# Performance work log

Hardware: AMD Instinct MI355X
Metric: run time of the kernel (lower is better)

The kernel has to match this reference:

```python
import jax, jax.numpy as jnp
import numpy as np

MAX_LEN = 3

def _attention(h, enc, w1, b1, w2):
    # h: [B,H], enc: [B,S,H]
    B, S, H = enc.shape
    hs = jnp.broadcast_to(h[:, None, :], (B, S, H))
    x = jnp.tanh(jnp.concatenate([enc, hs], axis=-1) @ w1.T + b1)  # [B,S,H]
    e = (x @ w2.T)[..., 0]                                         # [B,S]
    alpha = jax.nn.softmax(e, axis=1)
    return jnp.einsum('bs,bsd->bd', alpha, enc)                    # [B,H]

def _gru_cell(x, h, w_ih, w_hh, b_ih, b_hh):
    # torch GRU gate order: r, z, n
    H = h.shape[-1]
    gi = x @ w_ih.T + b_ih   # [B,3H]
    gh = h @ w_hh.T + b_hh
    i_r, i_z, i_n = gi[:, :H], gi[:, H:2*H], gi[:, 2*H:]
    h_r, h_z, h_n = gh[:, :H], gh[:, H:2*H], gh[:, 2*H:]
    r = jax.nn.sigmoid(i_r + h_r)
    z = jax.nn.sigmoid(i_z + h_z)
    n = jnp.tanh(i_n + r * h_n)
    return (1.0 - z) * n + z * h

def setup_inputs() -> dict:
    key = jax.random.key(0)
    ks = jax.random.split(key, 16)
    B, S, H, DW = 1024, 40, 1024, 512
    V0 = V1 = 4000
    EMB_N = V0 + V1 + 1
    sc = lambda fan: 1.0 / np.sqrt(fan)
    inp = {
        'encoder_outputs': jax.random.normal(ks[0], (B, S, H), jnp.float32),
        'encoder_hidden': jax.random.normal(ks[1], (1, B, H), jnp.float32),
        'targets': jax.random.randint(ks[2], (MAX_LEN, B), 0, V0),
        'emb': jax.random.normal(ks[3], (EMB_N, DW), jnp.float32) * 0.02,
        'attn_w1': jax.random.normal(ks[4], (H, 2 * H), jnp.float32) * sc(2 * H),
        'attn_b1': jnp.zeros((H,), jnp.float32),
        'attn_w2': jax.random.normal(ks[5], (1, H), jnp.float32) * sc(H),
        'w_ih': jax.random.normal(ks[6], (3 * H, H + DW), jnp.float32) * sc(H),
        'w_hh': jax.random.normal(ks[7], (3 * H, H), jnp.float32) * sc(H),
        'b_ih': jnp.zeros((3 * H,), jnp.float32),
        'b_hh': jnp.zeros((3 * H,), jnp.float32),
        'out0_w': jax.random.normal(ks[8], (V0, H), jnp.float32) * sc(H),
        'out0_b': jnp.zeros((V0,), jnp.float32),
        'out1_w': jax.random.normal(ks[9], (V1, H), jnp.float32) * sc(H),
        'out1_b': jnp.zeros((V1,), jnp.float32),
    }
    return inp

def reference(encoder_outputs, encoder_hidden, targets, emb, attn_w1, attn_b1,
              attn_w2, w_ih, w_hh, b_ih, b_hh, out0_w, out0_b, out1_w, out1_b):
    B = encoder_outputs.shape[0]
    h = encoder_hidden[0]  # n_layers=1, unidirectional -> init state passthrough
    logs = []
    for t in range(MAX_LEN):
        context = _attention(h, encoder_outputs, attn_w1, attn_b1, attn_w2)
        if t == 0:
            it = jnp.zeros((B,), jnp.int32)
        elif t == 1:
            it = targets[0] + 1
        else:
            it = targets[t - 1] + 36
        x = jnp.concatenate([emb[it], context], axis=1)  # [B, DW+H]
        h = _gru_cell(x, h, w_ih, w_hh, b_ih, b_hh)
        if t == 0 or t == 2:
            logits = h @ out0_w.T + out0_b
        else:
            logits = h @ out1_w.T + out1_b
        logs.append(jax.nn.log_softmax(logits, axis=1))
    return jnp.stack(logs)  # [MAX_LEN, B, V]
```

## Files before the change

kernel.cpp:

```cpp
#include <hip/hip_runtime.h>
#include <hip/hip_bf16.h>
#include <math.h>

#define B_SZ 1024
#define S_SZ 40
#define H_SZ 1024
#define DW_SZ 512
#define V_SZ 4000
#define XW (DW_SZ + H_SZ)
#define NGL 8192

typedef __bf16 bf16x8 __attribute__((ext_vector_type(8)));
typedef float f32x4 __attribute__((ext_vector_type(4)));
typedef unsigned short u16x8 __attribute__((ext_vector_type(8)));

__device__ __forceinline__ float fast_tanh(float x) {
    return 1.0f - 2.0f / (1.0f + __expf(2.0f * x));
}
__device__ __forceinline__ float fast_sigmoid(float x) {
    return 1.0f / (1.0f + __expf(-x));
}
__device__ __forceinline__ float bfraw2f(unsigned short u) {
    return __uint_as_float(((unsigned)u) << 16);
}
__device__ __forceinline__ ushort4 cvt4(float4 v) {
    union { ushort4 u; __hip_bfloat16 h[4]; } o;
    o.h[0] = __float2bfloat16(v.x); o.h[1] = __float2bfloat16(v.y);
    o.h[2] = __float2bfloat16(v.z); o.h[3] = __float2bfloat16(v.w);
    return o.u;
}
__device__ __forceinline__ u16x8 pack8(float4 a, float4 b) {
    union { u16x8 v; ushort4 h[2]; } o;
    o.h[0] = cvt4(a); o.h[1] = cvt4(b);
    return o.v;
}

#define GLL16(gp, lp)                                                                \
    __builtin_amdgcn_global_load_lds((const __attribute__((address_space(1))) void*)(gp), \
                                     (__attribute__((address_space(3))) void*)(lp), 16, 0, 0)

__device__ void cast_tail_block(int blk, int tid,
                                const float* __restrict__ w1, const float* __restrict__ whh,
                                const float* __restrict__ wih, const float* __restrict__ o0,
                                const float* __restrict__ o1,
                                __hip_bfloat16* __restrict__ wall0,
                                __hip_bfloat16* __restrict__ wall1,
                                __hip_bfloat16* __restrict__ wih_bf) {
    ushort4* w0u = reinterpret_cast<ushort4*>(wall0);
    ushort4* w1u = reinterpret_cast<ushort4*>(wall1);
    if (blk < 256) {
        const int r0 = blk * 4;
        const float4* s = reinterpret_cast<const float4*>(w1);
        ushort4 u0 = cvt4(s[(r0 + 0) * 512 + 256 + tid]), u1 = cvt4(s[(r0 + 1) * 512 + 256 + tid]),
                u2 = cvt4(s[(r0 + 2) * 512 + 256 + tid]), u3 = cvt4(s[(r0 + 3) * 512 + 256 + tid]);
        const int li = r0 * 256 + tid;
        w0u[li] = u0; w0u[li + 256] = u1; w0u[li + 512] = u2; w0u[li + 768] = u3;
        w1u[li] = u0; w1u[li + 256] = u1; w1u[li + 512] = u2; w1u[li + 768] = u3;
    } else if (blk < 1024) {
        const int li = (blk - 256) * 1024 + tid;
        const float4* s = reinterpret_cast<const float4*>(whh);
        ushort4 u0 = cvt4(s[li]), u1 = cvt4(s[li + 256]), u2 = cvt4(s[li + 512]), u3 = cvt4(s[li + 768]);
        w0u[262144 + li] = u0; w0u[262144 + li + 256] = u1;
        w0u[262144 + li + 512] = u2; w0u[262144 + li + 768] = u3;
        w1u[262144 + li] = u0; w1u[262144 + li + 256] = u1;
        w1u[262144 + li + 512] = u2; w1u[262144 + li + 768] = u3;
    } else if (blk < 2176) {
        const int li = (blk - 1024) * 1024 + tid;
        const float4* s = reinterpret_cast<const float4*>(wih);
        float4 v0 = s[li], v1 = s[li + 256], v2 = s[li + 512], v3 = s[li + 768];
        ushort4* d = reinterpret_cast<ushort4*>(wih_bf);
        d[li] = cvt4(v0); d[li + 256] = cvt4(v1); d[li + 512] = cvt4(v2); d[li + 768] = cvt4(v3);
    } else if (blk < 3176) {
        const int li = (blk - 2176) * 1024 + tid;
        const float4* s = reinterpret_cast<const float4*>(o0);
        float4 v0 = s[li], v1 = s[li + 256], v2 = s[li + 512], v3 = s[li + 768];
        w0u[1048576 + li] = cvt4(v0); w0u[1048576 + li + 256] = cvt4(v1);
        w0u[1048576 + li + 512] = cvt4(v2); w0u[1048576 + li + 768] = cvt4(v3);
    } else if (blk < 4176) {
        const int li = (blk - 3176) * 1024 + tid;
        const float4* s = reinterpret_cast<const float4*>(o1);
        float4 v0 = s[li], v1 = s[li + 256], v2 = s[li + 512], v3 = s[li + 768];
        w1u[1048576 + li] = cvt4(v0); w1u[1048576 + li + 256] = cvt4(v1);
        w1u[1048576 + li + 512] = cvt4(v2); w1u[1048576 + li + 768] = cvt4(v3);
    } else {
        const ushort4 z = make_ushort4(0, 0, 0, 0);
        if (blk < 4200) {
            const int li = 2072576 + (blk - 4176) * 1024 + tid;
            w0u[li] = z; w0u[li + 256] = z; w0u[li + 512] = z; w0u[li + 768] = z;
        } else {
            const int li = 2072576 + (blk - 4200) * 1024 + tid;
            w1u[li] = z; w1u[li + 256] = z; w1u[li + 512] = z; w1u[li + 768] = z;
        }
    }
}

__global__ __launch_bounds__(256, 2) void gemm_enc_cast(
    const __hip_bfloat16* __restrict__ A, int lda,
    const __hip_bfloat16* __restrict__ W, int ldw,
    __hip_bfloat16* __restrict__ C, int ldc,
    int nbx, int K, int gemm_nb,
    const float* __restrict__ w1, const float* __restrict__ whh,
    const float* __restrict__ wih, const float* __restrict__ o0,
    const float* __restrict__ o1,
    __hip_bfloat16* __restrict__ wall0, __hip_bfloat16* __restrict__ wall1,
    __hip_bfloat16* __restrict__ wih_bf) {
    extern __shared__ char smem[];
    const int tid = threadIdx.x;

    if ((int)blockIdx.x >= gemm_nb) {
        cast_tail_block(blockIdx.x - gemm_nb, tid, w1, whh, wih, o0, o1, wall0, wall1, wih_bf);
        return;
    }

    const int lane = tid & 63;
    const int wave = tid >> 6;
    const int wm = wave >> 1, wn = wave & 1;
    const int fr = lane & 15, fq = lane >> 4;

    int bid = blockIdx.x;
    { const int cpx = gemm_nb >> 3; bid = (bid & 7) * cpx + (bid >> 3); }
    const int by = bid / nbx;
    const int bm = by * 128;
    const int bn = (bid - by * nbx) * 256;

    const int r0 = tid >> 2;
    const int s0 = (tid & 3) ^ ((tid >> 3) & 3);
    const __hip_bfloat16* gA0 = A + (size_t)(bm + r0) * lda + s0 * 8;
    const __hip_bfloat16* gA1 = A + (size_t)(bm + r0 + 64) * lda + s0 * 8;
    const __hip_bfloat16* gW0 = W + (size_t)(bn + r0) * ldw + s0 * 8;
    const __hip_bfloat16* gW1 = W + (size_t)(bn + r0 + 64) * ldw + s0 * 8;
    const __hip_bfloat16* gW2 = W + (size_t)(bn + r0 + 128) * ldw + s0 * 8;
    const __hip_bfloat16* gW3 = W + (size_t)(bn + r0 + 192) * ldw + s0 * 8;
    const int dst0 = tid * 16;

    int aoff[4], boff[8];
#pragma unroll
    for (int mi = 0; mi < 4; ++mi) {
        const int row = wm * 64 + mi * 16 + fr;
        aoff[mi] = row * 64 + ((fq ^ ((row >> 1) & 3)) << 4);
    }
#pragma unroll
    for (int ni = 0; ni < 8; ++ni) {
        const int col = wn * 128 + ni * 16 + fr;
        boff[ni] = 8192 + col * 64 + ((fq ^ ((col >> 1) & 3)) << 4);
    }

    const int NT = K >> 5;
    f32x4 acc[4][8] = {};

#define STAGE_T(t)                                                    \
    do {                                                              \
        char* sb = smem + ((t) % 3) * 24576;                          \
        const int kk = (t) << 5;                                      \
        GLL16(gA0 + kk, sb + dst0);                                   \
        GLL16(gA1 + kk, sb + dst0 + 4096);                            \
        GLL16(gW0 + kk, sb + 8192 + dst0);                            \
        GLL16(gW1 + kk, sb + 8192 + dst0 + 4096);                     \
        GLL16(gW2 + kk, sb + 8192 + dst0 + 8192);                     \
        GLL16(gW3 + kk, sb + 8192 + dst0 + 12288);                    \
    } while (0)

    STAGE_T(0);
    STAGE_T(1);
    __builtin_amdgcn_sched_barrier(0);
    asm volatile("s_waitcnt vmcnt(6)" ::: "memory");
    __builtin_amdgcn_s_barrier();
    __builtin_amdgcn_sched_barrier(0);

    for (int t = 0; t < NT; ++t) {
        const char* sb = smem + (t % 3) * 24576;
        bf16x8 af[4], bg[8];
#pragma unroll
        for (int ni = 0; ni < 8; ++ni) bg[ni] = *reinterpret_cast<const bf16x8*>(sb + boff[ni]);
#pragma unroll
        for (int mi = 0; mi < 4; ++mi) af[mi] = *reinterpret_cast<const bf16x8*>(sb + aoff[mi]);

        if (t + 2 < NT) STAGE_T(t + 2);

        __builtin_amdgcn_s_setprio(1);
#pragma unroll
        for (int mi = 0; mi < 4; ++mi)
#pragma unroll
            for (int ni = 0; ni < 8; ++ni)
                acc[mi][ni] = __builtin_amdgcn_mfma_f32_16x16x32_bf16(af[mi], bg[ni], acc[mi][ni], 0, 0, 0);
        __builtin_amdgcn_s_setprio(0);

        if (t != NT - 1) {
            __builtin_amdgcn_sched_barrier(0);
            if (t + 2 < NT) asm volatile("s_waitcnt vmcnt(6)" ::: "memory");
            else            asm volatile("s_waitcnt vmcnt(0)" ::: "memory");
            __builtin_amdgcn_s_barrier();
            __builtin_amdgcn_sched_barrier(0);
        }
    }
#undef STAGE_T

#pragma unroll
    for (int ni = 0; ni < 8; ++ni) {
        const int col = bn + wn * 128 + ni * 16 + fr;
#pragma unroll
        for (int mi = 0; mi < 4; ++mi) {
            const int row0 = bm + wm * 64 + mi * 16 + fq * 4;
#pragma unroll
            for (int r = 0; r < 4; ++r)
                C[(size_t)(row0 + r) * ldc + col] = __float2bfloat16(acc[mi][ni][r]);
        }
    }
}

__global__ __launch_bounds__(512, 2) void gemm_bt_pipe128_v2(
    const __hip_bfloat16* __restrict__ A, int lda,
    const __hip_bfloat16* __restrict__ W, int ldw,
    const float* __restrict__ bias,
    __hip_bfloat16* __restrict__ C, int ldc,
    int nbx, int K) {
    extern __shared__ char smem[];
    const int tid = threadIdx.x;
    const int lane = tid & 63;
    const int wave = tid >> 6;
    const int wm = wave >> 2, wn = wave & 3;
    const int fr = lane & 15, fq = lane >> 4;

    int bid = blockIdx.x;
    { const int cpx = gridDim.x >> 3; bid = (bid & 7) * cpx + (bid >> 3); }
    const int by = bid / nbx;
    const int bm = by * 128;
    const int bn = (bid - by * nbx) * 256;

    const int r0 = tid >> 2;
    const int s0 = (tid & 3) ^ ((tid >> 3) & 3);
    const __hip_bfloat16* gA0 = A + (size_t)(bm + r0) * lda + s0 * 8;
    const __hip_bfloat16* gW0 = W + (size_t)(bn + r0) * ldw + s0 * 8;
    const __hip_bfloat16* gW1 = W + (size_t)(bn + r0 + 128) * ldw + s0 * 8;
    const int dst0 = tid * 16;

    int aoff[4], boff[4];
#pragma unroll
    for (int mi = 0; mi < 4; ++mi) {
        const int row = wm * 64 + mi * 16 + fr;
        aoff[mi] = row * 64 + ((fq ^ ((row >> 1) & 3)) << 4);
    }
#pragma unroll
    for (int ni = 0; ni < 4; ++ni) {
        const int col = wn * 64 + ni * 16 + fr;
        boff[ni] = 8192 + col * 64 + ((fq ^ ((col >> 1) & 3)) << 4);
    }

    const int NT = K >> 5;
    f32x4 acc[4][4] = {};

#define STAGE_T(t)                                                    \
    do {                                                              \
        char* sb = smem + ((t) % 3) * 24576;                          \
        const int kk = (t) << 5;                                      \
        GLL16(gA0 + kk, sb + dst0);                                   \
        GLL16(gW0 + kk, sb + 8192 + dst0);                            \
        GLL16(gW1 + kk, sb + 8192 + dst0 + 8192);                     \
    } while (0)

    STAGE_T(0);
    STAGE_T(1);
    __builtin_amdgcn_sched_barrier(0);
    asm volatile("s_waitcnt vmcnt(3)" ::: "memory");
    __builtin_amdgcn_s_barrier();
    __builtin_amdgcn_sched_barrier(0);

    for (int t = 0; t < NT; ++t) {
        const char* sb = smem + (t % 3) * 24576;
        bf16x8 af[4], bg[4];
#pragma unroll
        for (int ni = 0; ni < 4; ++ni) bg[ni] = *reinterpret_cast<const bf16x8*>(sb + boff[ni]);
#pragma unroll
        for (int mi = 0; mi < 4; ++mi) af[mi] = *reinterpret_cast<const bf16x8*>(sb + aoff[mi]);

        if (t + 2 < NT) STAGE_T(t + 2);

        __builtin_amdgcn_s_setprio(1);
#pragma unroll
        for (int mi = 0; mi < 4; ++mi)
#pragma unroll
            for (int ni = 0; ni < 4; ++ni)
                acc[mi][ni] = __builtin_amdgcn_mfma_f32_16x16x32_bf16(af[mi], bg[ni], acc[mi][ni], 0, 0, 0);
        __builtin_amdgcn_s_setprio(0);

        if (t != NT - 1) {
            __builtin_amdgcn_sched_barrier(0);
            if (t + 2 < NT) asm volatile("s_waitcnt vmcnt(3)" ::: "memory");
            else            asm volatile("s_waitcnt vmcnt(0)" ::: "memory");
            __builtin_amdgcn_s_barrier();
            __builtin_amdgcn_sched_barrier(0);
        }
    }
#undef STAGE_T

#pragma unroll
    for (int ni = 0; ni < 4; ++ni) {
        const int col = bn + wn * 64 + ni * 16 + fr;
        const float bb = bias ? bias[col] : 0.0f;
#pragma unroll
        for (int mi = 0; mi < 4; ++mi) {
            const int row0 = bm + wm * 64 + mi * 16 + fq * 4;
#pragma unroll
            for (int r = 0; r < 4; ++r)
                C[(size_t)(row0 + r) * ldc + col] = __float2bfloat16(acc[mi][ni][r] + bb);
        }
    }
}

#define PA_ENC 10240
#define PA_W1A (PA_ENC + 256)
#define PA_EMB (PA_W1A + 3072)
#define PA_H   (PA_EMB + 1024)
#define PA_TOT (PA_H + 2)
__global__ __launch_bounds__(256) void prep_a_kernel(
    const float* __restrict__ enc, const float* __restrict__ w1,
    __hip_bfloat16* __restrict__ enc_bf, __hip_bfloat16* __restrict__ w1a_bf,
    const float* __restrict__ emb, const int* __restrict__ targets,
    __hip_bfloat16* __restrict__ x0, __hip_bfloat16* __restrict__ x1, __hip_bfloat16* __restrict__ x2,
    const float* __restrict__ enc_h, float* __restrict__ h, __hip_bfloat16* __restrict__ h_bf,
    const float* __restrict__ b1, const float* __restrict__ b_hh,
    const float* __restrict__ o0b, const float* __restrict__ o1b,
    float* __restrict__ bias0, float* __restrict__ bias1) {
    const int blk = blockIdx.x;
    const int tid = threadIdx.x;

    if (blk < PA_ENC) {
        const float4* s = reinterpret_cast<const float4*>(enc);
        u16x8* d = reinterpret_cast<u16x8*>(enc_bf);
        const int f0 = blk * 1024 + tid * 2;
        const int f1 = f0 + 512;
        float4 a0 = s[f0], a1 = s[f0 + 1];
        float4 b0 = s[f1], b1v = s[f1 + 1];
        d[blk * 512 + tid] = pack8(a0, a1);
        d[blk * 512 + 256 + tid] = pack8(b0, b1v);
    } else if (blk < PA_W1A) {
        const int r0 = (blk - PA_ENC) * 4;
        const float4* s = reinterpret_cast<const float4*>(w1);
        float4 v0 = s[(r0 + 0) * 512 + tid], v1 = s[(r0 + 1) * 512 + tid],
               v2 = s[(r0 + 2) * 512 + tid], v3 = s[(r0 + 3) * 512 + tid];
        ushort4* d = reinterpret_cast<ushort4*>(w1a_bf);
        const int li = r0 * 256 + tid;
        d[li] = cvt4(v0); d[li + 256] = cvt4(v1); d[li + 512] = cvt4(v2); d[li + 768] = cvt4(v3);
    } else if (blk < PA_EMB) {
        if (tid >= 128) return;
        const int e = blk - PA_W1A;
        const int t = e >> 10;
        const int b = e & 1023;
        int it; __hip_bfloat16* x;
        if (t == 0) { it = 0; x = x0; }
        else if (t == 1) { it = targets[b] + 1; x = x1; }
        else { it = targets[B_SZ + b] + 36; x = x2; }
        float4 v = reinterpret_cast<const float4*>(emb + (size_t)it * DW_SZ)[tid];
        reinterpret_cast<ushort4*>(x + (size_t)b * XW)[tid] = cvt4(v);
    } else if (blk < PA_H) {
        const int i = (blk - PA_EMB) * 256 + tid;
        const float4 v = reinterpret_cast<const float4*>(enc_h)[i];
        reinterpret_cast<float4*>(h)[i] = v;
        reinterpret_cast<ushort4*>(h_bf)[i] = cvt4(v);
    } else {
        float* bt = (blk == PA_H) ? bias0 : bias1;
        const float* ob = (blk == PA_H) ? o0b : o1b;
        for (int j = tid; j < NGL; j += 256) {
            float v;
            if (j < H_SZ) v = b1[j];
            else if (j < 4 * H_SZ) v = b_hh[j - H_SZ];
            else if (j < 4 * H_SZ + V_SZ) v = ob[j - 4 * H_SZ];
            else v = 0.0f;
            bt[j] = v;
        }
    }
}

__global__ __launch_bounds__(256) void attn_ls_kernel(
    const __hip_bfloat16* __restrict__ enc,
    const __hip_bfloat16* __restrict__ enc_proj,
    const __hip_bfloat16* __restrict__ hgl,
    const float* __restrict__ w2,
    __hip_bfloat16* __restrict__ x,
    float* __restrict__ outp,
    int nattn) {
    const int blk = blockIdx.x;
    const int tid = threadIdx.x;
    const int lane = tid & 63, wave = tid >> 6;
    __shared__ float s_e[S_SZ];
    __shared__ float s_red[4];
    __shared__ float s_bc;

    if (blk < nattn) {
        const int b = blk;
        float hp[16], wv[16];
        const unsigned short* hgrow = reinterpret_cast<const unsigned short*>(hgl) + (size_t)b * NGL;
#pragma unroll
        for (int p = 0; p < 4; ++p) {
            const int base = p * 256 + lane * 4;
            ushort4 hu = *reinterpret_cast<const ushort4*>(hgrow + base);
            float4 wq = *reinterpret_cast<const float4*>(w2 + base);
            hp[p * 4 + 0] = bfraw2f(hu.x); hp[p * 4 + 1] = bfraw2f(hu.y);
            hp[p * 4 + 2] = bfraw2f(hu.z); hp[p * 4 + 3] = bfraw2f(hu.w);
            wv[p * 4 + 0] = wq.x; wv[p * 4 + 1] = wq.y;
            wv[p * 4 + 2] = wq.z; wv[p * 4 + 3] = wq.w;
        }

        const unsigned short* ep0 = reinterpret_cast<const unsigned short*>(enc_proj) + (size_t)b * S_SZ * H_SZ;
#pragma unroll 2
        for (int i = 0; i < 10; ++i) {
            const int s = wave + 4 * i;
            const unsigned short* row = ep0 + (size_t)s * H_SZ;
            float acc = 0.f;
#pragma unroll
            for (int p = 0; p < 4; ++p) {
                ushort4 eu = *reinterpret_cast<const ushort4*>(row + p * 256 + lane * 4);
                acc += fast_tanh(bfraw2f(eu.x) + hp[p * 4 + 0]) * wv[p * 4 + 0]
                     + fast_tanh(bfraw2f(eu.y) + hp[p * 4 + 1]) * wv[p * 4 + 1]
                     + fast_tanh(bfraw2f(eu.z) + hp[p * 4 + 2]) * wv[p * 4 + 2]
                     + fast_tanh(bfraw2f(eu.w) + hp[p * 4 + 3]) * wv[p * 4 + 3];
            }
#pragma unroll
            for (int off = 32; off > 0; off >>= 1) acc += __shfl_down(acc, off);
            if (lane == 0) s_e[s] = acc;
        }
        __syncthreads();

        float m = -1e30f;
        for (int s = 0; s < S_SZ; ++s) m = fmaxf(m, s_e[s]);
        float sum = 0.f;
        for (int s = 0; s < S_SZ; ++s) sum += __expf(s_e[s] - m);
        const float inv = 1.0f / sum;

        const ushort4* enc_b = reinterpret_cast<const ushort4*>(enc + (size_t)b * S_SZ * H_SZ);
        float4 acc = make_float4(0.f, 0.f, 0.f, 0.f);
        for (int s = 0; s < S_SZ; ++s) {
            const float a = __expf(s_e[s] - m) * inv;
            ushort4 ev = enc_b[s * 256 + tid];
            acc.x += a * bfraw2f(ev.x); acc.y += a * bfraw2f(ev.y);
            acc.z += a * bfraw2f(ev.z); acc.w += a * bfraw2f(ev.w);
        }
        reinterpret_cast<ushort4*>(x + (size_t)b * XW + DW_SZ)[tid] = cvt4(acc);
    } else {
        const int b = blk - nattn;
        const ushort4* row4 = reinterpret_cast<const ushort4*>(
            reinterpret_cast<const unsigned short*>(hgl) + (size_t)b * NGL + 4096);
        float* orow = outp + (size_t)b * V_SZ;

        float m = -1e30f;
        for (int k = tid; k < V_SZ / 4; k += 256) {
            ushort4 u = row4[k];
            m = fmaxf(m, fmaxf(fmaxf(bfraw2f(u.x), bfraw2f(u.y)), fmaxf(bfraw2f(u.z), bfraw2f(u.w))));
        }
#pragma unroll
        for (int off = 32; off > 0; off >>= 1) m = fmaxf(m, __shfl_down(m, off));
        if (lane == 0) s_red[wave] = m;
        __syncthreads();
        if (tid == 0) s_bc = fmaxf(fmaxf(s_red[0], s_red[1]), fmaxf(s_red[2], s_red[3]));
        __syncthreads();
        m = s_bc;

        float sum = 0.f;
        for (int k = tid; k < V_SZ / 4; k += 256) {
            ushort4 u = row4[k];
            sum += expf(bfraw2f(u.x) - m) + expf(bfraw2f(u.y) - m)
                 + expf(bfraw2f(u.z) - m) + expf(bfraw2f(u.w) - m);
        }
#pragma unroll
        for (int off = 32; off > 0; off >>= 1) sum += __shfl_down(sum, off);
        __syncthreads();
        if (lane == 0) s_red[wave] = sum;
        __syncthreads();
        if (tid == 0) s_bc = logf(s_red[0] + s_red[1] + s_red[2] + s_red[3]) + m;
        __syncthreads();
        const float ls = s_bc;

        for (int k = tid; k < V_SZ / 4; k += 256) {
            ushort4 u = row4[k];
            float4 o = make_float4(bfraw2f(u.x) - ls, bfraw2f(u.y) - ls,
                                   bfraw2f(u.z) - ls, bfraw2f(u.w) - ls);
            reinterpret_cast<float4*>(orow)[k] = o;
        }
    }
}

__global__ __launch_bounds__(256) void gru_gate_kernel(
    const __hip_bfloat16* __restrict__ gi,
    const __hip_bfloat16* __restrict__ hgl,
    float* __restrict__ h,
    __hip_bfloat16* __restrict__ h_bf) {
    const int idx = blockIdx.x * 256 + threadIdx.x;
    const int b = idx >> 10;
    const int j = idx & 1023;
    const unsigned short* gib = reinterpret_cast<const unsigned short*>(gi) + (size_t)b * 3 * H_SZ;
    const unsigned short* ghb = reinterpret_cast<const unsigned short*>(hgl) + (size_t)b * NGL + H_SZ;
    const float i_r = bfraw2f(gib[j]), i_z = bfraw2f(gib[H_SZ + j]), i_n = bfraw2f(gib[2 * H_SZ + j]);
    const float h_r = bfraw2f(ghb[j]), h_z = bfraw2f(ghb[H_SZ + j]), h_n = bfraw2f(ghb[2 * H_SZ + j]);
    const float r = fast_sigmoid(i_r + h_r);
    const float z = fast_sigmoid(i_z + h_z);
    const float n = fast_tanh(i_n + r * h_n);
    const float hv = (1.0f - z) * n + z * h[idx];
    h[idx] = hv;
    h_bf[idx] = __float2bfloat16(hv);
}

extern "C" void kernel_launch(void* const* d_in, const int* in_sizes, int n_in,
                              void* d_out, int out_size, void* d_ws, size_t ws_size,
                              hipStream_t stream) {
    const float* enc    = (const float*)d_in[0];
    const float* enc_h  = (const float*)d_in[1];
    const int*   tgt    = (const int*)d_in[2];
    const float* emb    = (const float*)d_in[3];
    const float* w1     = (const float*)d_in[4];
    const float* b1     = (const float*)d_in[5];
    const float* w2     = (const float*)d_in[6];
    const float* w_ih   = (const float*)d_in[7];
    const float* w_hh   = (const float*)d_in[8];
    const float* b_ih   = (const float*)d_in[9];
    const float* b_hh   = (const float*)d_in[10];
    const float* out0_w = (const float*)d_in[11];
    const float* out0_b = (const float*)d_in[12];
    const float* out1_w = (const float*)d_in[13];
    const float* out1_b = (const float*)d_in[14];
    float* out = (float*)d_out;

    char* wp = (char*)d_ws;
    auto carve = [&](size_t bytes) { char* p = wp; wp += (bytes + 255) & ~(size_t)255; return p; };
    __hip_bfloat16* enc_bf  = (__hip_bfloat16*)carve((size_t)B_SZ * S_SZ * H_SZ * 2);
    __hip_bfloat16* encp_bf = (__hip_bfloat16*)carve((size_t)B_SZ * S_SZ * H_SZ * 2);
    __hip_bfloat16* w1a_bf  = (__hip_bfloat16*)carve((size_t)H_SZ * H_SZ * 2);
    __hip_bfloat16* wall0   = (__hip_bfloat16*)carve((size_t)NGL * H_SZ * 2);
    __hip_bfloat16* wall1   = (__hip_bfloat16*)carve((size_t)NGL * H_SZ * 2);
    __hip_bfloat16* wih_bf  = (__hip_bfloat16*)carve((size_t)3 * H_SZ * XW * 2);
    float*          bias0   = (float*)carve((size_t)NGL * 4);
    float*          bias1   = (float*)carve((size_t)NGL * 4);
    float*          h       = (float*)carve((size_t)B_SZ * H_SZ * 4);
    __hip_bfloat16* h_bf    = (__hip_bfloat16*)carve((size_t)B_SZ * H_SZ * 2);
    __hip_bfloat16* hgl     = (__hip_bfloat16*)carve((size_t)B_SZ * NGL * 2);
    __hip_bfloat16* x_bf[3];
    for (int t = 0; t < 3; ++t) x_bf[t] = (__hip_bfloat16*)carve((size_t)B_SZ * XW * 2);
    __hip_bfloat16* gi_bf   = (__hip_bfloat16*)carve((size_t)B_SZ * 3 * H_SZ * 2);

    prep_a_kernel<<<PA_TOT, 256, 0, stream>>>(enc, w1, enc_bf, w1a_bf,
                                              emb, tgt, x_bf[0], x_bf[1], x_bf[2],
                                              enc_h, h, h_bf, b1, b_hh, out0_b, out1_b,
                                              bias0, bias1);

    const int gemm_nb = (B_SZ * S_SZ / 128) * (H_SZ / 256);
    gemm_enc_cast<<<gemm_nb + 4224, 256, 3 * 24576, stream>>>(
        enc_bf, H_SZ, w1a_bf, H_SZ, encp_bf, H_SZ, H_SZ / 256, H_SZ, gemm_nb,
        w1, w_hh, w_ih, out0_w, out1_w, wall0, wall1, wih_bf);

    gemm_bt_pipe128_v2<<<(B_SZ / 128) * 16, 512, 3 * 24576, stream>>>(
        h_bf, H_SZ, wall0, H_SZ, bias0, hgl, NGL, 16, H_SZ);

    attn_ls_kernel<<<B_SZ, 256, 0, stream>>>(enc_bf, encp_bf, hgl, w2, x_bf[0], out, B_SZ);

    for (int t = 0; t < 3; ++t) {
        gemm_bt_pipe128_v2<<<(B_SZ / 128) * 12, 512, 3 * 24576, stream>>>(
            x_bf[t], XW, wih_bf, XW, b_ih, gi_bf, 3 * H_SZ, 12, XW);

        gru_gate_kernel<<<(B_SZ * H_SZ) / 256, 256, 0, stream>>>(gi_bf, hgl, h, h_bf);

        if (t == 0) {
            gemm_bt_pipe128_v2<<<(B_SZ / 128) * 32, 512, 3 * 24576, stream>>>(
                h_bf, H_SZ, wall0, H_SZ, bias0, hgl, NGL, 32, H_SZ);
        } else if (t == 1) {
            gemm_bt_pipe128_v2<<<(B_SZ / 128) * 32, 512, 3 * 24576, stream>>>(
                h_bf, H_SZ, wall1, H_SZ, bias1, hgl, NGL, 32, H_SZ);
        } else {
            gemm_bt_pipe128_v2<<<(B_SZ / 128) * 16, 512, 3 * 24576, stream>>>(
                h_bf, H_SZ, wall0 + (size_t)4 * H_SZ * H_SZ, H_SZ, bias0 + 4 * H_SZ,
                hgl + 4 * H_SZ, NGL, 16, H_SZ);
        }

        float* outp = out + (size_t)t * B_SZ * V_SZ;
        if (t < 2) {
            attn_ls_kernel<<<2 * B_SZ, 256, 0, stream>>>(enc_bf, encp_bf, hgl, w2, x_bf[t + 1],
                                                         outp, B_SZ);
        } else {
            attn_ls_kernel<<<B_SZ, 256, 0, stream>>>(enc_bf, encp_bf, hgl, w2, x_bf[0],
                                                     outp, 0);
        }
    }
}
```

Baseline: 479.7 us.

## Fuse fp32-to-bf16 encoder cast into projection GEMM A-tile loads

Removes the separate pass that converted encoder_outputs to bf16 (and its workspace buffer). The encoder GEMM now loads fp32 A tiles into registers, converts them and writes bf16 to LDS, software-pipelined across a ping-pong register set, while W keeps direct global-to-LDS loads. Attention now reads fp32 encoder outputs directly, which avoids the cast but doubles the bytes it reads per pass. The trade is saving a 160MB read plus an 80MB write against higher register pressure and more load traffic in the GEMM and the attention kernels.

```diff
diff --git a/kernel.cpp b/kernel.cpp
--- a/kernel.cpp
+++ b/kernel.cpp
@@ -38,6 +38,9 @@
 #define GLL16(gp, lp)                                                                \
     __builtin_amdgcn_global_load_lds((const __attribute__((address_space(1))) void*)(gp), \
                                      (__attribute__((address_space(3))) void*)(lp), 16, 0, 0)
+#define SBAR0 __builtin_amdgcn_sched_barrier(0)
+#define WAITVM(n) asm volatile("s_waitcnt vmcnt(" #n ")" ::: "memory")
+#define WAITLG0 asm volatile("s_waitcnt lgkmcnt(0)" ::: "memory")
 
 __device__ void cast_tail_block(int blk, int tid,
                                 const float* __restrict__ w1, const float* __restrict__ whh,
@@ -94,8 +97,8 @@
     }
 }
 
-__global__ __launch_bounds__(256, 2) void gemm_enc_cast(
-    const __hip_bfloat16* __restrict__ A, int lda,
+__global__ __launch_bounds__(256, 2) void gemm_f32a_cast(
+    const float* __restrict__ Af, int lda,
     const __hip_bfloat16* __restrict__ W, int ldw,
     __hip_bfloat16* __restrict__ C, int ldc,
     int nbx, int K, int gemm_nb,
@@ -125,8 +128,8 @@
 
     const int r0 = tid >> 2;
     const int s0 = (tid & 3) ^ ((tid >> 3) & 3);
-    const __hip_bfloat16* gA0 = A + (size_t)(bm + r0) * lda + s0 * 8;
-    const __hip_bfloat16* gA1 = A + (size_t)(bm + r0 + 64) * lda + s0 * 8;
+    const float* gAf0 = Af + (size_t)(bm + r0) * lda + s0 * 8;
+    const float* gAf1 = Af + (size_t)(bm + r0 + 64) * lda + s0 * 8;
     const __hip_bfloat16* gW0 = W + (size_t)(bn + r0) * ldw + s0 * 8;
     const __hip_bfloat16* gW1 = W + (size_t)(bn + r0 + 64) * ldw + s0 * 8;
     const __hip_bfloat16* gW2 = W + (size_t)(bn + r0 + 128) * ldw + s0 * 8;
@@ -147,53 +150,95 @@
 
     const int NT = K >> 5;
     f32x4 acc[4][8] = {};
-
-#define STAGE_T(t)                                                    \
+    float4 pa0, pa1, pa2, pa3, pb0, pb1, pb2, pb3;
+
+#define STAGEB(t)                                                     \
     do {                                                              \
-        char* sb = smem + ((t) % 3) * 24576;                          \
+        char* sw = smem + ((t) % 3) * 24576;                          \
         const int kk = (t) << 5;                                      \
-        GLL16(gA0 + kk, sb + dst0);                                   \
-        GLL16(gA1 + kk, sb + dst0 + 4096);                            \
-        GLL16(gW0 + kk, sb + 8192 + dst0);                            \
-        GLL16(gW1 + kk, sb + 8192 + dst0 + 4096);                     \
-        GLL16(gW2 + kk, sb + 8192 + dst0 + 8192);                     \
-        GLL16(gW3 + kk, sb + 8192 + dst0 + 12288);                    \
+        GLL16(gW0 + kk, sw + 8192 + dst0);                            \
+        GLL16(gW1 + kk, sw + 8192 + dst0 + 4096);                     \
+        GLL16(gW2 + kk, sw + 8192 + dst0 + 8192);                     \
+        GLL16(gW3 + kk, sw + 8192 + dst0 + 12288);                    \
     } while (0)
-
-    STAGE_T(0);
-    STAGE_T(1);
-    __builtin_amdgcn_sched_barrier(0);
-    asm volatile("s_waitcnt vmcnt(6)" ::: "memory");
+#define LOADA(t, q0, q1, q2, q3)                                      \
+    do {                                                              \
+        const int kk = (t) << 5;                                      \
+        q0 = *reinterpret_cast<const float4*>(gAf0 + kk);             \
+        q1 = *reinterpret_cast<const float4*>(gAf0 + kk + 4);         \
+        q2 = *reinterpret_cast<const float4*>(gAf1 + kk);             \
+        q3 = *reinterpret_cast<const float4*>(gAf1 + kk + 4);         \
+    } while (0)
+#define WRITEA(t, q0, q1, q2, q3)                                     \
+    do {                                                              \
+        char* sw = smem + ((t) % 3) * 24576;                          \
+        *reinterpret_cast<u16x8*>(sw + dst0) = pack8(q0, q1);         \
+        *reinterpret_cast<u16x8*>(sw + dst0 + 4096) = pack8(q2, q3);  \
+    } while (0)
+#define FRAGS(t)                                                      \
+    const char* sb = smem + ((t) % 3) * 24576;                        \
+    bf16x8 af[4], bg[8];                                              \
+    _Pragma("unroll")                                                 \
+    for (int ni = 0; ni < 8; ++ni) bg[ni] = *reinterpret_cast<const bf16x8*>(sb + boff[ni]); \
+    _Pragma("unroll")                                                 \
+    for (int mi = 0; mi < 4; ++mi) af[mi] = *reinterpret_cast<const bf16x8*>(sb + aoff[mi]);
+#define MFMA32                                                        \
+    __builtin_amdgcn_s_setprio(1);                                    \
+    _Pragma("unroll")                                                 \
+    for (int mi = 0; mi < 4; ++mi)                                    \
+    _Pragma("unroll")                                                 \
+        for (int ni = 0; ni < 8; ++ni)                                \
+            acc[mi][ni] = __builtin_amdgcn_mfma_f32_16x16x32_bf16(af[mi], bg[ni], acc[mi][ni], 0, 0, 0); \
+    __builtin_amdgcn_s_setprio(0);
+
+    STAGEB(0); LOADA(0, pa0, pa1, pa2, pa3);
+    STAGEB(1); LOADA(1, pb0, pb1, pb2, pb3);
+    SBAR0; WAITVM(8); SBAR0;
+    WRITEA(0, pa0, pa1, pa2, pa3);
+    WAITLG0; SBAR0;
     __builtin_amdgcn_s_barrier();
-    __builtin_amdgcn_sched_barrier(0);
-
-    for (int t = 0; t < NT; ++t) {
-        const char* sb = smem + (t % 3) * 24576;
-        bf16x8 af[4], bg[8];
-#pragma unroll
-        for (int ni = 0; ni < 8; ++ni) bg[ni] = *reinterpret_cast<const bf16x8*>(sb + boff[ni]);
-#pragma unroll
-        for (int mi = 0; mi < 4; ++mi) af[mi] = *reinterpret_cast<const bf16x8*>(sb + aoff[mi]);
-
-        if (t + 2 < NT) STAGE_T(t + 2);
-
-        __builtin_amdgcn_s_setprio(1);
-#pragma unroll
-        for (int mi = 0; mi < 4; ++mi)
-#pragma unroll
-            for (int ni = 0; ni < 8; ++ni)
-                acc[mi][ni] = __builtin_amdgcn_mfma_f32_16x16x32_bf16(af[mi], bg[ni], acc[mi][ni], 0, 0, 0);
-        __builtin_amdgcn_s_setprio(0);
-
-        if (t != NT - 1) {
-            __builtin_amdgcn_sched_barrier(0);
-            if (t + 2 < NT) asm volatile("s_waitcnt vmcnt(6)" ::: "memory");
-            else            asm volatile("s_waitcnt vmcnt(0)" ::: "memory");
+    SBAR0;
+
+    for (int tt = 0; tt < NT - 2; tt += 2) {
+        {
+            FRAGS(tt);
+            STAGEB(tt + 2); LOADA(tt + 2, pa0, pa1, pa2, pa3);
+            MFMA32;
+            SBAR0; WAITVM(8); SBAR0;
+            WRITEA(tt + 1, pb0, pb1, pb2, pb3);
+            WAITLG0; SBAR0;
             __builtin_amdgcn_s_barrier();
-            __builtin_amdgcn_sched_barrier(0);
-        }
-    }
-#undef STAGE_T
+            SBAR0;
+        }
+        {
+            FRAGS(tt + 1);
+            STAGEB(tt + 3); LOADA(tt + 3, pb0, pb1, pb2, pb3);
+            MFMA32;
+            SBAR0; WAITVM(8); SBAR0;
+            WRITEA(tt + 2, pa0, pa1, pa2, pa3);
+            WAITLG0; SBAR0;
+            __builtin_amdgcn_s_barrier();
+            SBAR0;
+        }
+    }
+    {
+        FRAGS(NT - 2);
+        MFMA32;
+        SBAR0; WAITVM(0); SBAR0;
+        WRITEA(NT - 1, pb0, pb1, pb2, pb3);
+        WAITLG0; SBAR0;
+        __builtin_amdgcn_s_barrier();
+        SBAR0;
+    }
+    {
+        FRAGS(NT - 1);
+        MFMA32;
+    }
+#undef STAGEB
+#undef LOADA
+#undef WRITEA
+#undef FRAGS
+#undef MFMA32
 
 #pragma unroll
     for (int ni = 0; ni < 8; ++ni) {
@@ -260,10 +305,10 @@
 
     STAGE_T(0);
     STAGE_T(1);
-    __builtin_amdgcn_sched_barrier(0);
-    asm volatile("s_waitcnt vmcnt(3)" ::: "memory");
+    SBAR0;
+    WAITVM(3);
     __builtin_amdgcn_s_barrier();
-    __builtin_amdgcn_sched_barrier(0);
+    SBAR0;
 
     for (int t = 0; t < NT; ++t) {
         const char* sb = smem + (t % 3) * 24576;
@@ -284,11 +329,11 @@
         __builtin_amdgcn_s_setprio(0);
 
         if (t != NT - 1) {
-            __builtin_amdgcn_sched_barrier(0);
-            if (t + 2 < NT) asm volatile("s_waitcnt vmcnt(3)" ::: "memory");
-            else            asm volatile("s_waitcnt vmcnt(0)" ::: "memory");
+            SBAR0;
+            if (t + 2 < NT) WAITVM(3);
+            else            WAITVM(0);
             __builtin_amdgcn_s_barrier();
-            __builtin_amdgcn_sched_barrier(0);
+            SBAR0;
         }
     }
 #undef STAGE_T
@@ -307,14 +352,12 @@
     }
 }
 
-#define PA_ENC 10240
-#define PA_W1A (PA_ENC + 256)
+#define PA_W1A 256
 #define PA_EMB (PA_W1A + 3072)
 #define PA_H   (PA_EMB + 1024)
 #define PA_TOT (PA_H + 2)
 __global__ __launch_bounds__(256) void prep_a_kernel(
-    const float* __restrict__ enc, const float* __restrict__ w1,
-    __hip_bfloat16* __restrict__ enc_bf, __hip_bfloat16* __restrict__ w1a_bf,
+    const float* __restrict__ w1, __hip_bfloat16* __restrict__ w1a_bf,
     const float* __restrict__ emb, const int* __restrict__ targets,
     __hip_bfloat16* __restrict__ x0, __hip_bfloat16* __restrict__ x1, __hip_bfloat16* __restrict__ x2,
     const float* __restrict__ enc_h, float* __restrict__ h, __hip_bfloat16* __restrict__ h_bf,
@@ -324,17 +367,8 @@
     const int blk = blockIdx.x;
     const int tid = threadIdx.x;
 
-    if (blk < PA_ENC) {
-        const float4* s = reinterpret_cast<const float4*>(enc);
-        u16x8* d = reinterpret_cast<u16x8*>(enc_bf);
-        const int f0 = blk * 1024 + tid * 2;
-        const int f1 = f0 + 512;
-        float4 a0 = s[f0], a1 = s[f0 + 1];
-        float4 b0 = s[f1], b1v = s[f1 + 1];
-        d[blk * 512 + tid] = pack8(a0, a1);
-        d[blk * 512 + 256 + tid] = pack8(b0, b1v);
-    } else if (blk < PA_W1A) {
-        const int r0 = (blk - PA_ENC) * 4;
+    if (blk < PA_W1A) {
+        const int r0 = blk * 4;
         const float4* s = reinterpret_cast<const float4*>(w1);
         float4 v0 = s[(r0 + 0) * 512 + tid], v1 = s[(r0 + 1) * 512 + tid],
                v2 = s[(r0 + 2) * 512 + tid], v3 = s[(r0 + 3) * 512 + tid];
@@ -372,7 +406,7 @@
 }
 
 __global__ __launch_bounds__(256) void attn_ls_kernel(
-    const __hip_bfloat16* __restrict__ enc,
+    const float* __restrict__ enc,
     const __hip_bfloat16* __restrict__ enc_proj,
     const __hip_bfloat16* __restrict__ hgl,
     const float* __restrict__ w2,
@@ -427,13 +461,13 @@
         for (int s = 0; s < S_SZ; ++s) sum += __expf(s_e[s] - m);
         const float inv = 1.0f / sum;
 
-        const ushort4* enc_b = reinterpret_cast<const ushort4*>(enc + (size_t)b * S_SZ * H_SZ);
+        const float4* enc_b = reinterpret_cast<const float4*>(enc + (size_t)b * S_SZ * H_SZ);
         float4 acc = make_float4(0.f, 0.f, 0.f, 0.f);
         for (int s = 0; s < S_SZ; ++s) {
             const float a = __expf(s_e[s] - m) * inv;
-            ushort4 ev = enc_b[s * 256 + tid];
-            acc.x += a * bfraw2f(ev.x); acc.y += a * bfraw2f(ev.y);
-            acc.z += a * bfraw2f(ev.z); acc.w += a * bfraw2f(ev.w);
+            float4 ev = enc_b[s * 256 + tid];
+            acc.x += a * ev.x; acc.y += a * ev.y;
+            acc.z += a * ev.z; acc.w += a * ev.w;
         }
         reinterpret_cast<ushort4*>(x + (size_t)b * XW + DW_SZ)[tid] = cvt4(acc);
     } else {
@@ -521,7 +555,6 @@
 
     char* wp = (char*)d_ws;
     auto carve = [&](size_t bytes) { char* p = wp; wp += (bytes + 255) & ~(size_t)255; return p; };
-    __hip_bfloat16* enc_bf  = (__hip_bfloat16*)carve((size_t)B_SZ * S_SZ * H_SZ * 2);
     __hip_bfloat16* encp_bf = (__hip_bfloat16*)carve((size_t)B_SZ * S_SZ * H_SZ * 2);
     __hip_bfloat16* w1a_bf  = (__hip_bfloat16*)carve((size_t)H_SZ * H_SZ * 2);
     __hip_bfloat16* wall0   = (__hip_bfloat16*)carve((size_t)NGL * H_SZ * 2);
@@ -536,20 +569,20 @@
     for (int t = 0; t < 3; ++t) x_bf[t] = (__hip_bfloat16*)carve((size_t)B_SZ * XW * 2);
     __hip_bfloat16* gi_bf   = (__hip_bfloat16*)carve((size_t)B_SZ * 3 * H_SZ * 2);
 
-    prep_a_kernel<<<PA_TOT, 256, 0, stream>>>(enc, w1, enc_bf, w1a_bf,
+    prep_a_kernel<<<PA_TOT, 256, 0, stream>>>(w1, w1a_bf,
                                               emb, tgt, x_bf[0], x_bf[1], x_bf[2],
                                               enc_h, h, h_bf, b1, b_hh, out0_b, out1_b,
                                               bias0, bias1);
 
     const int gemm_nb = (B_SZ * S_SZ / 128) * (H_SZ / 256);
-    gemm_enc_cast<<<gemm_nb + 4224, 256, 3 * 24576, stream>>>(
-        enc_bf, H_SZ, w1a_bf, H_SZ, encp_bf, H_SZ, H_SZ / 256, H_SZ, gemm_nb,
+    gemm_f32a_cast<<<gemm_nb + 4224, 256, 3 * 24576, stream>>>(
+        enc, H_SZ, w1a_bf, H_SZ, encp_bf, H_SZ, H_SZ / 256, H_SZ, gemm_nb,
         w1, w_hh, w_ih, out0_w, out1_w, wall0, wall1, wih_bf);
 
     gemm_bt_pipe128_v2<<<(B_SZ / 128) * 16, 512, 3 * 24576, stream>>>(
         h_bf, H_SZ, wall0, H_SZ, bias0, hgl, NGL, 16, H_SZ);
 
-    attn_ls_kernel<<<B_SZ, 256, 0, stream>>>(enc_bf, encp_bf, hgl, w2, x_bf[0], out, B_SZ);
+    attn_ls_kernel<<<B_SZ, 256, 0, stream>>>(enc, encp_bf, hgl, w2, x_bf[0], out, B_SZ);
 
     for (int t = 0; t < 3; ++t) {
         gemm_bt_pipe128_v2<<<(B_SZ / 128) * 12, 512, 3 * 24576, stream>>>(
@@ -571,10 +604,10 @@
 
         float* outp = out + (size_t)t * B_SZ * V_SZ;
         if (t < 2) {
-            attn_ls_kernel<<<2 * B_SZ, 256, 0, stream>>>(enc_bf, encp_bf, hgl, w2, x_bf[t + 1],
+            attn_ls_kernel<<<2 * B_SZ, 256, 0, stream>>>(enc, encp_bf, hgl, w2, x_bf[t + 1],
                                                          outp, B_SZ);
         } else {
-            attn_ls_kernel<<<B_SZ, 256, 0, stream>>>(enc_bf, encp_bf, hgl, w2, x_bf[0],
+            attn_ls_kernel<<<B_SZ, 256, 0, stream>>>(enc, encp_bf, hgl, w2, x_bf[0],
                                                      outp, 0);
         }
     }
```

Result: slower. 546.6 us (+13.9%).
